# Optimization experiments

Hardware: AMD Instinct MI355X
Metric: run time of the kernel (lower is better)

The kernel has to match this reference:

```python
import jax, jax.numpy as jnp
import numpy as np

K_NUM = 4      # kernel_num: size of dynamic kernel bank
KS = 3         # spatial kernel size


def _fdconv(x, w_fr, w_fi, b, a1w, a1b, a2w, a2b):
    """Frequency-dynamic conv: kernels parameterized in the Fourier domain,
    mixed per-sample by a GAP->MLP->softmax attention over the kernel bank,
    then applied as a per-sample 3x3 conv (batched via grouped conv).
    x: [B,Cin,H,W]; w_fr/w_fi: [K,Cout,Cin,3,2] (rfft2 coeffs); b: [Cout]."""
    B, Cin, H, W = x.shape
    # per-sample kernel attention
    gap = x.mean((2, 3))                                   # [B,Cin]
    h = jax.nn.relu(gap @ a1w + a1b)                       # [B,hidden]
    attn = jax.nn.softmax(h @ a2w + a2b, axis=-1)          # [B,K]
    # synthesize spatial kernels from frequency coefficients
    w = jnp.fft.irfft2(w_fr + 1j * w_fi, s=(KS, KS), axes=(-2, -1))  # [K,Co,Ci,3,3]
    w = w.astype(x.dtype)
    wd = jnp.einsum('bk,koihw->boihw', attn, w)            # [B,Co,Ci,3,3]
    Co = wd.shape[1]
    # per-sample conv via feature_group_count=B grouped conv
    xg = x.reshape(1, B * Cin, H, W)
    wg = wd.reshape(B * Co, Cin, KS, KS)
    y = jax.lax.conv_general_dilated(
        xg, wg, window_strides=(1, 1), padding='SAME',
        dimension_numbers=('NCHW', 'OIHW', 'NCHW'),
        feature_group_count=B)
    return y.reshape(B, Co, H, W) + b[None, :, None, None]


def setup_inputs() -> dict:
    key = jax.random.key(0)
    ks = jax.random.split(key, 16)
    B, Cin, Cout, H, W = 16, 128, 256, 128, 128
    h1, h2 = Cin // 4, Cout // 4
    FR = KS // 2 + 1  # rfft bins along last dim
    s = 0.05
    return {
        'x': jax.random.normal(ks[0], (B, Cin, H, W), jnp.float32),
        # conv1 (Cin->Cout)
        'w1_fr': jax.random.normal(ks[1], (K_NUM, Cout, Cin, KS, FR), jnp.float32) * s,
        'w1_fi': jax.random.normal(ks[2], (K_NUM, Cout, Cin, KS, FR), jnp.float32) * s,
        'b1': jnp.zeros((Cout,), jnp.float32),
        'a1w1': jax.random.normal(ks[3], (Cin, h1), jnp.float32) * s,
        'a1b1': jnp.zeros((h1,), jnp.float32),
        'a1w2': jax.random.normal(ks[4], (h1, K_NUM), jnp.float32) * s,
        'a1b2': jnp.zeros((K_NUM,), jnp.float32),
        # conv2 (Cout->Cout)
        'w2_fr': jax.random.normal(ks[5], (K_NUM, Cout, Cout, KS, FR), jnp.float32) * s,
        'w2_fi': jax.random.normal(ks[6], (K_NUM, Cout, Cout, KS, FR), jnp.float32) * s,
        'b2': jnp.zeros((Cout,), jnp.float32),
        'a2w1': jax.random.normal(ks[7], (Cout, h2), jnp.float32) * s,
        'a2b1': jnp.zeros((h2,), jnp.float32),
        'a2w2': jax.random.normal(ks[8], (h2, K_NUM), jnp.float32) * s,
        'a2b2': jnp.zeros((K_NUM,), jnp.float32),
    }


def reference(x, w1_fr, w1_fi, b1, a1w1, a1b1, a1w2, a1b2,
              w2_fr, w2_fi, b2, a2w1, a2b1, a2w2, a2b2):
    y = jax.nn.relu(_fdconv(x, w1_fr, w1_fi, b1, a1w1, a1b1, a1w2, a1b2))
    y = jax.nn.relu(_fdconv(y, w2_fr, w2_fi, b2, a2w1, a2b1, a2w2, a2b2))
    return y
```

## Files before the change

kernel.cpp:

```cpp
#include <hip/hip_runtime.h>
#include <hip/hip_bf16.h>
#include <math.h>


#define K_NUM 4
typedef __attribute__((ext_vector_type(8))) short short8;
typedef __attribute__((ext_vector_type(4))) float f32x4;

__device__ inline float bf2f(short s) {
  unsigned u = ((unsigned)(unsigned short)s) << 16;
  return __uint_as_float(u);
}
__device__ inline short f2bf(float f) {
  __hip_bfloat16 h = __float2bfloat16(f);
  return (short)*reinterpret_cast<unsigned short*>(&h);
}

__global__ void fd_gap_kernel(const float* __restrict__ x, float* __restrict__ out, int HW) {
  const float4* p = (const float4*)(x + (size_t)blockIdx.x * HW);
  int n4 = HW >> 2;
  float s = 0.f;
  for (int i = threadIdx.x; i < n4; i += blockDim.x) {
    float4 v = p[i];
    s += v.x + v.y + v.z + v.w;
  }
  for (int off = 32; off > 0; off >>= 1) s += __shfl_down(s, off, 64);
  __shared__ float wsum[4];
  int lane = threadIdx.x & 63, w = threadIdx.x >> 6;
  if (lane == 0) wsum[w] = s;
  __syncthreads();
  if (threadIdx.x == 0) {
    float t = 0.f;
    int nw = blockDim.x >> 6;
    for (int i = 0; i < nw; ++i) t += wsum[i];
    out[blockIdx.x] = t / (float)HW;
  }
}

__global__ __launch_bounds__(1024) void gap_t_part_kernel(
    const short* __restrict__ y, float* __restrict__ part) {
  const int HW = 16384, CO = 256;
  int b = blockIdx.y, ch = blockIdx.x;
  int t = threadIdx.x;
  int tg = t & 31, pg = t >> 5;
  const short* base = y + ((size_t)b * HW + (size_t)ch * 1024) * CO + tg * 8;
  float s[8];
#pragma unroll
  for (int j = 0; j < 8; ++j) s[j] = 0.f;
  for (int px = pg; px < 1024; px += 32) {
    short8 v = *(const short8*)(base + (size_t)px * CO);
#pragma unroll
    for (int j = 0; j < 8; ++j) s[j] += bf2f(v[j]);
  }
  __shared__ float red[32][32][8];
#pragma unroll
  for (int j = 0; j < 8; ++j) red[pg][tg][j] = s[j];
  __syncthreads();
  if (t < 256) {
    float tot = 0.f;
    const float* r = (const float*)red;
#pragma unroll
    for (int p = 0; p < 32; ++p) tot += r[p * 256 + t];
    part[((size_t)b * 16 + ch) * 256 + t] = tot;
  }
}
__global__ void gap_t_reduce_kernel(const float* __restrict__ part, float* __restrict__ gap) {
  int b = blockIdx.x, co = threadIdx.x;
  float s = 0.f;
  for (int c = 0; c < 16; ++c) s += part[(b * 16 + c) * 256 + co];
  gap[b * 256 + co] = s * (1.f / 16384.f);
}

__global__ void fd_attn_kernel(const float* __restrict__ gap, int C, int Hd,
                               const float* __restrict__ w1, const float* __restrict__ b1,
                               const float* __restrict__ w2, const float* __restrict__ b2,
                               float* __restrict__ attn) {
  int b = blockIdx.x, j = threadIdx.x;
  __shared__ float h[64];
  __shared__ float z[K_NUM];
  if (j < Hd) {
    float s = b1[j];
    const float* g = gap + (size_t)b * C;
    for (int c = 0; c < C; ++c) s = fmaf(g[c], w1[c * Hd + j], s);
    h[j] = fmaxf(s, 0.f);
  }
  __syncthreads();
  if (j < K_NUM) {
    float s = b2[j];
    for (int c = 0; c < Hd; ++c) s = fmaf(h[c], w2[c * K_NUM + j], s);
    z[j] = s;
  }
  __syncthreads();
  if (j == 0) {
    float m = z[0];
    for (int k = 1; k < K_NUM; ++k) m = fmaxf(m, z[k]);
    float e[K_NUM], sum = 0.f;
    for (int k = 0; k < K_NUM; ++k) { e[k] = expf(z[k] - m); sum += e[k]; }
    for (int k = 0; k < K_NUM; ++k) attn[b * K_NUM + k] = e[k] / sum;
  }
}

__global__ void fd_synth_t_kernel(const float* __restrict__ wfr, const float* __restrict__ wfi,
                                  const float* __restrict__ attn, short* __restrict__ wdt,
                                  int B, int CO, int CI) {
  size_t gid = (size_t)blockIdx.x * blockDim.x + threadIdx.x;
  size_t total = (size_t)B * CI * CO;
  if (gid >= total) return;
  int ci = (int)(gid % CI);
  size_t t = gid / CI;
  int co = (int)(t % CO);
  int b = (int)(t / CO);

  float a[K_NUM];
  for (int k = 0; k < K_NUM; ++k) a[k] = attn[b * K_NUM + k];

  float Fr[3][2], Fi[3][2];
  for (int u = 0; u < 3; ++u) for (int v = 0; v < 2; ++v) { Fr[u][v] = 0.f; Fi[u][v] = 0.f; }
  for (int k = 0; k < K_NUM; ++k) {
    size_t base = ((((size_t)k * CO + co) * CI + ci) * 3) * 2;
    const float* pr = wfr + base;
    const float* pi = wfi + base;
    float ak = a[k];
    for (int u = 0; u < 3; ++u)
      for (int v = 0; v < 2; ++v) {
        Fr[u][v] = fmaf(ak, pr[u * 2 + v], Fr[u][v]);
        Fi[u][v] = fmaf(ak, pi[u * 2 + v], Fi[u][v]);
      }
  }

  const float CS[3] = {1.f, -0.5f, -0.5f};
  const float SN[3] = {0.f, 0.8660254037844386f, -0.8660254037844386f};
  float outv[9];
  for (int ai = 0; ai < 3; ++ai) {
    float Gr[2], Gi[2];
    for (int v = 0; v < 2; ++v) {
      float gr = 0.f, gi = 0.f;
      for (int u = 0; u < 3; ++u) {
        int idx = (u * ai) % 3;
        gr += Fr[u][v] * CS[idx] - Fi[u][v] * SN[idx];
        gi += Fr[u][v] * SN[idx] + Fi[u][v] * CS[idx];
      }
      Gr[v] = gr * (1.f / 3.f);
      Gi[v] = gi * (1.f / 3.f);
    }
    for (int bi = 0; bi < 3; ++bi)
      outv[ai * 3 + bi] = (Gr[0] + 2.f * (Gr[1] * CS[bi] - Gi[1] * SN[bi])) * (1.f / 3.f);
  }
  int ci8 = ci >> 3, cil = ci & 7;
  for (int s = 0; s < 9; ++s)
    wdt[((((size_t)b * 9 + s) * (CI / 8) + ci8) * CO + co) * 8 + cil] = f2bf(outv[s]);
}

__global__ __launch_bounds__(256) void transpose_bf16_kernel(
    const float* __restrict__ in, short* __restrict__ out, int C) {
  const int HW = 16384;
  __shared__ short t[64 * 40];
  int tid = threadIdx.x;
  int px0 = blockIdx.x * 64, c0 = blockIdx.y * 32, b = blockIdx.z;
  int px = tid & 63, cb = tid >> 6;
#pragma unroll
  for (int i = 0; i < 8; ++i) {
    int c = i * 4 + cb;
    float v = in[((size_t)b * C + c0 + c) * HW + px0 + px];
    t[px * 40 + c] = f2bf(v);
  }
  __syncthreads();
  int px2 = tid >> 2, g = tid & 3;
  short8 v = *(const short8*)(t + px2 * 40 + g * 8);
  *(short8*)(out + ((size_t)b * HW + px0 + px2) * C + c0 + g * 8) = v;
}

template <int CI, int MODE>
__global__ __launch_bounds__(512) void conv_mfma_kernel(
    const short* __restrict__ xin,
    const short* __restrict__ wdt,
    const float* __restrict__ bias,
    short* __restrict__ yout_t,
    float* __restrict__ yout_f) {
  const int H = 128, W = 128, HW = H * W, CO = 256;
  const int NKC = CI / 32;
  __shared__ short xs[2][18 * 18 * 40];

  const int tid = threadIdx.x;
  const int w = tid >> 6;
  const int wy = w & 3, wc = w >> 2;
  const int lane = tid & 63;
  const int l15 = lane & 15, l4 = lane >> 4;
  const int tx0 = (blockIdx.x & 7) * 16, ty0 = (blockIdx.x >> 3) * 16;
  const int cob = blockIdx.y * 128 + wc * 64;
  const int b = blockIdx.z;

  int sr[3], sc[3], sg[3];
#pragma unroll
  for (int i = 0; i < 3; ++i) {
    int idx = i * 512 + tid;
    int pxi = idx >> 2;
    sg[i] = idx & 3;
    sr[i] = pxi / 18;
    sc[i] = pxi - sr[i] * 18;
  }
  const bool has2 = (tid < 272);

  short8 pre[3];
  auto stage_load = [&](int kc) {
#pragma unroll
    for (int i = 0; i < 3; ++i) {
      if (i < 2 || has2) {
        int gy = ty0 + sr[i] - 1, gx = tx0 + sc[i] - 1;
        short8 v = {0, 0, 0, 0, 0, 0, 0, 0};
        if ((unsigned)gy < (unsigned)H && (unsigned)gx < (unsigned)W)
          v = *(const short8*)(xin + ((size_t)b * HW + gy * W + gx) * CI + kc * 32 + sg[i] * 8);
        pre[i] = v;
      }
    }
  };
  auto stage_write = [&](short* buf) {
#pragma unroll
    for (int i = 0; i < 3; ++i) {
      if (i < 2 || has2) {
        int pxi = sr[i] * 18 + sc[i];
        *(short8*)(buf + pxi * 40 + sg[i] * 8) = pre[i];
      }
    }
  };

  f32x4 acc[4][4];
#pragma unroll
  for (int i = 0; i < 4; ++i)
#pragma unroll
    for (int j = 0; j < 4; ++j)
      acc[i][j] = (f32x4){0.f, 0.f, 0.f, 0.f};

  stage_load(0);
  stage_write(xs[0]);
  __syncthreads();

  int cur = 0;
  for (int kc = 0; kc < NKC; ++kc) {
    const bool more = (kc + 1 < NKC);
    if (more) stage_load(kc + 1);
    const short* bufc = xs[cur];

#pragma unroll
    for (int dc = 0; dc < 3; ++dc) {
      short8 xf[6];
#pragma unroll
      for (int rr = 0; rr < 6; ++rr)
        xf[rr] = *(const short8*)(bufc + ((4 * wy + rr) * 18 + l15 + dc) * 40 + l4 * 8);
      short8 wf[3][4];
#pragma unroll
      for (int dr = 0; dr < 3; ++dr) {
        const short* wp = wdt + ((((size_t)b * 9 + dr * 3 + dc) * (CI / 8) + kc * 4 + l4) * CO + cob + l15) * 8;
#pragma unroll
        for (int cf = 0; cf < 4; ++cf)
          wf[dr][cf] = *(const short8*)(wp + cf * 128);
      }
#pragma unroll
      for (int dr = 0; dr < 3; ++dr)
#pragma unroll
        for (int nf = 0; nf < 4; ++nf)
#pragma unroll
          for (int cf = 0; cf < 4; ++cf) {
            if (MODE == 0)
              acc[nf][cf] = __builtin_amdgcn_mfma_f32_16x16x32_bf16(
                  xf[nf + dr], wf[dr][cf], acc[nf][cf], 0, 0, 0);
            else
              acc[nf][cf] = __builtin_amdgcn_mfma_f32_16x16x32_bf16(
                  wf[dr][cf], xf[nf + dr], acc[nf][cf], 0, 0, 0);
          }
    }

    if (more) stage_write(xs[cur ^ 1]);
    __syncthreads();
    cur ^= 1;
  }

  if (MODE == 0) {
#pragma unroll
    for (int cf = 0; cf < 4; ++cf) {
      float bs = bias[cob + cf * 16 + l15];
#pragma unroll
      for (int nf = 0; nf < 4; ++nf) {
        int row = ty0 + 4 * wy + nf;
#pragma unroll
        for (int r = 0; r < 4; ++r) {
          int col = tx0 + l4 * 4 + r;
          float v = fmaxf(acc[nf][cf][r] + bs, 0.f);
          yout_t[((size_t)b * HW + (size_t)row * W + col) * CO + cob + cf * 16 + l15] = f2bf(v);
        }
      }
    }
  } else {
#pragma unroll
    for (int cf = 0; cf < 4; ++cf) {
#pragma unroll
      for (int r = 0; r < 4; ++r) {
        int co = cob + cf * 16 + l4 * 4 + r;
        float bs = bias[co];
#pragma unroll
        for (int nf = 0; nf < 4; ++nf) {
          int row = ty0 + 4 * wy + nf;
          int col = tx0 + l15;
          yout_f[((size_t)b * CO + co) * HW + (size_t)row * W + col] =
              fmaxf(acc[nf][cf][r] + bs, 0.f);
        }
      }
    }
  }
}

extern "C" void kernel_launch(void* const* d_in, const int* in_sizes, int n_in,
                              void* d_out, int out_size, void* d_ws, size_t ws_size,
                              hipStream_t stream) {
  const int B = 16, CIN = 128, COUT = 256, H = 128, W = 128, HW = H * W;

  const float* x    = (const float*)d_in[0];
  const float* w1fr = (const float*)d_in[1];
  const float* w1fi = (const float*)d_in[2];
  const float* b1   = (const float*)d_in[3];
  const float* a1w1 = (const float*)d_in[4];
  const float* a1b1 = (const float*)d_in[5];
  const float* a1w2 = (const float*)d_in[6];
  const float* a1b2 = (const float*)d_in[7];
  const float* w2fr = (const float*)d_in[8];
  const float* w2fi = (const float*)d_in[9];
  const float* b2   = (const float*)d_in[10];
  const float* a2w1 = (const float*)d_in[11];
  const float* a2b1 = (const float*)d_in[12];
  const float* a2w2 = (const float*)d_in[13];
  const float* a2b2 = (const float*)d_in[14];
  float* outf = (float*)d_out;

  short* xt = (short*)d_out;

  char* wsb = (char*)d_ws;
  short* y1t  = (short*)wsb;
  short* wdt  = (short*)(wsb + 134217728);
  float* gprt = (float*)(wsb + 134217728 + 18874368);
  float* gap  = (float*)(wsb + 134217728 + 18874368 + 262144);
  float* attn = (float*)(wsb + 134217728 + 18874368 + 262144 + 16384);

  transpose_bf16_kernel<<<dim3(HW / 64, CIN / 32, B), 256, 0, stream>>>(x, xt, CIN);
  fd_gap_kernel<<<B * CIN, 256, 0, stream>>>(x, gap, HW);
  fd_attn_kernel<<<B, 64, 0, stream>>>(gap, CIN, CIN / 4, a1w1, a1b1, a1w2, a1b2, attn);
  fd_synth_t_kernel<<<(B * CIN * COUT) / 256, 256, 0, stream>>>(w1fr, w1fi, attn, wdt, B, COUT, CIN);
  conv_mfma_kernel<128, 0><<<dim3(64, 2, 16), 512, 0, stream>>>(xt, wdt, b1, y1t, nullptr);

  gap_t_part_kernel<<<dim3(16, B), 1024, 0, stream>>>(y1t, gprt);
  gap_t_reduce_kernel<<<B, 256, 0, stream>>>(gprt, gap);
  fd_attn_kernel<<<B, 64, 0, stream>>>(gap, COUT, COUT / 4, a2w1, a2b1, a2w2, a2b2, attn);
  fd_synth_t_kernel<<<(B * COUT * COUT) / 256, 256, 0, stream>>>(w2fr, w2fi, attn, wdt, B, COUT, COUT);
  conv_mfma_kernel<256, 1><<<dim3(64, 2, 16), 512, 0, stream>>>(y1t, wdt, b2, nullptr, outf);
}
```

Before: 1.042 ms.

## Fuse global average pooling partial sums into transpose and conv1 epilogue

Computes per-channel partial sums for the attention GAP inside the input transpose kernel and inside the first conv's epilogue, then reduces them with a small kernel. This removes the separate full passes over x and over the conv1 output that existed only to compute means. Partial sums are staged in unused space of the output buffer, and the added shuffles and strided partial-sum writes add some epilogue cost.

```diff
diff --git a/kernel.cpp b/kernel.cpp
--- a/kernel.cpp
+++ b/kernel.cpp
@@ -16,59 +16,15 @@
   return (short)*reinterpret_cast<unsigned short*>(&h);
 }
 
-__global__ void fd_gap_kernel(const float* __restrict__ x, float* __restrict__ out, int HW) {
-  const float4* p = (const float4*)(x + (size_t)blockIdx.x * HW);
-  int n4 = HW >> 2;
-  float s = 0.f;
-  for (int i = threadIdx.x; i < n4; i += blockDim.x) {
-    float4 v = p[i];
-    s += v.x + v.y + v.z + v.w;
-  }
-  for (int off = 32; off > 0; off >>= 1) s += __shfl_down(s, off, 64);
-  __shared__ float wsum[4];
-  int lane = threadIdx.x & 63, w = threadIdx.x >> 6;
-  if (lane == 0) wsum[w] = s;
-  __syncthreads();
-  if (threadIdx.x == 0) {
-    float t = 0.f;
-    int nw = blockDim.x >> 6;
-    for (int i = 0; i < nw; ++i) t += wsum[i];
-    out[blockIdx.x] = t / (float)HW;
-  }
-}
-
-__global__ __launch_bounds__(1024) void gap_t_part_kernel(
-    const short* __restrict__ y, float* __restrict__ part) {
-  const int HW = 16384, CO = 256;
-  int b = blockIdx.y, ch = blockIdx.x;
-  int t = threadIdx.x;
-  int tg = t & 31, pg = t >> 5;
-  const short* base = y + ((size_t)b * HW + (size_t)ch * 1024) * CO + tg * 8;
-  float s[8];
-#pragma unroll
-  for (int j = 0; j < 8; ++j) s[j] = 0.f;
-  for (int px = pg; px < 1024; px += 32) {
-    short8 v = *(const short8*)(base + (size_t)px * CO);
-#pragma unroll
-    for (int j = 0; j < 8; ++j) s[j] += bf2f(v[j]);
-  }
-  __shared__ float red[32][32][8];
-#pragma unroll
-  for (int j = 0; j < 8; ++j) red[pg][tg][j] = s[j];
-  __syncthreads();
-  if (t < 256) {
-    float tot = 0.f;
-    const float* r = (const float*)red;
-#pragma unroll
-    for (int p = 0; p < 32; ++p) tot += r[p * 256 + t];
-    part[((size_t)b * 16 + ch) * 256 + t] = tot;
-  }
-}
-__global__ void gap_t_reduce_kernel(const float* __restrict__ part, float* __restrict__ gap) {
-  int b = blockIdx.x, co = threadIdx.x;
-  float s = 0.f;
-  for (int c = 0; c < 16; ++c) s += part[(b * 16 + c) * 256 + co];
-  gap[b * 256 + co] = s * (1.f / 16384.f);
+__global__ __launch_bounds__(256) void gap_reduce_kernel(
+    const float* __restrict__ part, float* __restrict__ gap, float scale) {
+  int row = blockIdx.x * 4 + (threadIdx.x >> 6);
+  int lane = threadIdx.x & 63;
+  float4 v = *(const float4*)(part + (size_t)row * 256 + lane * 4);
+  float s = v.x + v.y + v.z + v.w;
+#pragma unroll
+  for (int m = 1; m <= 32; m <<= 1) s += __shfl_xor(s, m, 64);
+  if (lane == 0) gap[row] = s * scale;
 }
 
 __global__ void fd_attn_kernel(const float* __restrict__ gap, int C, int Hd,
@@ -152,22 +108,33 @@
 }
 
 __global__ __launch_bounds__(256) void transpose_bf16_kernel(
-    const float* __restrict__ in, short* __restrict__ out, int C) {
+    const float* __restrict__ in, short* __restrict__ out, int C,
+    float* __restrict__ gpart1) {
   const int HW = 16384;
   __shared__ short t[64 * 40];
   int tid = threadIdx.x;
   int px0 = blockIdx.x * 64, c0 = blockIdx.y * 32, b = blockIdx.z;
   int px = tid & 63, cb = tid >> 6;
+  float sums[8];
 #pragma unroll
   for (int i = 0; i < 8; ++i) {
     int c = i * 4 + cb;
     float v = in[((size_t)b * C + c0 + c) * HW + px0 + px];
     t[px * 40 + c] = f2bf(v);
+    sums[i] = v;
   }
   __syncthreads();
   int px2 = tid >> 2, g = tid & 3;
   short8 v = *(const short8*)(t + px2 * 40 + g * 8);
   *(short8*)(out + ((size_t)b * HW + px0 + px2) * C + c0 + g * 8) = v;
+#pragma unroll
+  for (int m = 1; m <= 32; m <<= 1)
+#pragma unroll
+    for (int i = 0; i < 8; ++i) sums[i] += __shfl_xor(sums[i], m, 64);
+  if ((tid & 63) == 0)
+#pragma unroll
+    for (int i = 0; i < 8; ++i)
+      gpart1[((size_t)b * C + c0 + i * 4 + cb) * 256 + blockIdx.x] = sums[i];
 }
 
 template <int CI, int MODE>
@@ -176,7 +143,8 @@
     const short* __restrict__ wdt,
     const float* __restrict__ bias,
     short* __restrict__ yout_t,
-    float* __restrict__ yout_f) {
+    float* __restrict__ yout_f,
+    float* __restrict__ gpart2) {
   const int H = 128, W = 128, HW = H * W, CO = 256;
   const int NKC = CI / 32;
   __shared__ short xs[2][18 * 18 * 40];
@@ -276,6 +244,9 @@
   }
 
   if (MODE == 0) {
+    float gs[4];
+#pragma unroll
+    for (int cf = 0; cf < 4; ++cf) gs[cf] = 0.f;
 #pragma unroll
     for (int cf = 0; cf < 4; ++cf) {
       float bs = bias[cob + cf * 16 + l15];
@@ -286,9 +257,21 @@
         for (int r = 0; r < 4; ++r) {
           int col = tx0 + l4 * 4 + r;
           float v = fmaxf(acc[nf][cf][r] + bs, 0.f);
+          gs[cf] += v;
           yout_t[((size_t)b * HW + (size_t)row * W + col) * CO + cob + cf * 16 + l15] = f2bf(v);
         }
       }
+    }
+#pragma unroll
+    for (int cf = 0; cf < 4; ++cf) {
+      gs[cf] += __shfl_xor(gs[cf], 16, 64);
+      gs[cf] += __shfl_xor(gs[cf], 32, 64);
+    }
+    if (l4 == 0) {
+      int pslot = blockIdx.x * 4 + wy;
+#pragma unroll
+      for (int cf = 0; cf < 4; ++cf)
+        gpart2[((size_t)b * 256 + cob + cf * 16 + l15) * 256 + pslot] = gs[cf];
     }
   } else {
 #pragma unroll
@@ -331,24 +314,27 @@
   const float* a2b2 = (const float*)d_in[14];
   float* outf = (float*)d_out;
 
-  short* xt = (short*)d_out;
+  short* xt     = (short*)d_out;
+  float* gpart1 = (float*)((char*)d_out + 67108864);
+  float* gpart2 = (float*)((char*)d_out + 69206016);
 
   char* wsb = (char*)d_ws;
   short* y1t  = (short*)wsb;
   short* wdt  = (short*)(wsb + 134217728);
-  float* gprt = (float*)(wsb + 134217728 + 18874368);
-  float* gap  = (float*)(wsb + 134217728 + 18874368 + 262144);
-  float* attn = (float*)(wsb + 134217728 + 18874368 + 262144 + 16384);
-
-  transpose_bf16_kernel<<<dim3(HW / 64, CIN / 32, B), 256, 0, stream>>>(x, xt, CIN);
-  fd_gap_kernel<<<B * CIN, 256, 0, stream>>>(x, gap, HW);
-  fd_attn_kernel<<<B, 64, 0, stream>>>(gap, CIN, CIN / 4, a1w1, a1b1, a1w2, a1b2, attn);
+  float* gap1 = (float*)(wsb + 134217728 + 18874368);
+  float* gap2 = (float*)(wsb + 134217728 + 18874368 + 8192);
+  float* attn = (float*)(wsb + 134217728 + 18874368 + 8192 + 16384);
+
+  const float gsc = 1.f / (float)HW;
+
+  transpose_bf16_kernel<<<dim3(HW / 64, CIN / 32, B), 256, 0, stream>>>(x, xt, CIN, gpart1);
+  gap_reduce_kernel<<<(B * CIN) / 4, 256, 0, stream>>>(gpart1, gap1, gsc);
+  fd_attn_kernel<<<B, 64, 0, stream>>>(gap1, CIN, CIN / 4, a1w1, a1b1, a1w2, a1b2, attn);
   fd_synth_t_kernel<<<(B * CIN * COUT) / 256, 256, 0, stream>>>(w1fr, w1fi, attn, wdt, B, COUT, CIN);
-  conv_mfma_kernel<128, 0><<<dim3(64, 2, 16), 512, 0, stream>>>(xt, wdt, b1, y1t, nullptr);
-
-  gap_t_part_kernel<<<dim3(16, B), 1024, 0, stream>>>(y1t, gprt);
-  gap_t_reduce_kernel<<<B, 256, 0, stream>>>(gprt, gap);
-  fd_attn_kernel<<<B, 64, 0, stream>>>(gap, COUT, COUT / 4, a2w1, a2b1, a2w2, a2b2, attn);
+  conv_mfma_kernel<128, 0><<<dim3(64, 2, 16), 512, 0, stream>>>(xt, wdt, b1, y1t, nullptr, gpart2);
+
+  gap_reduce_kernel<<<(B * COUT) / 4, 256, 0, stream>>>(gpart2, gap2, gsc);
+  fd_attn_kernel<<<B, 64, 0, stream>>>(gap2, COUT, COUT / 4, a2w1, a2b1, a2w2, a2b2, attn);
   fd_synth_t_kernel<<<(B * COUT * COUT) / 256, 256, 0, stream>>>(w2fr, w2fi, attn, wdt, B, COUT, COUT);
-  conv_mfma_kernel<256, 1><<<dim3(64, 2, 16), 512, 0, stream>>>(y1t, wdt, b2, nullptr, outf);
-}
+  conv_mfma_kernel<256, 1><<<dim3(64, 2, 16), 512, 0, stream>>>(y1t, wdt, b2, nullptr, outf, nullptr);
+}
```

New measurement: 1.007 ms. 3.3% less time.
